# Kernel tuning notes

Measured on AMD Instinct MI355X. Metric: run time of the kernel, lower is better.

The kernel has to match this reference:

```python
import jax, jax.numpy as jnp
import numpy as np

N_NODES = 50000
N_EDGES = 800000
D = 128  # node_feat_size == edge_hidden_size


def setup_inputs() -> dict:
    key = jax.random.key(0)
    ks = jax.random.split(key, 10)
    return {
        "edge_logits": jax.random.normal(ks[0], (N_EDGES, 1), jnp.float32),
        "node_feats": jax.random.normal(ks[1], (N_NODES, D), jnp.float32),
        "src": jax.random.randint(ks[2], (N_EDGES,), 0, N_NODES),
        "dst": jax.random.randint(ks[3], (N_EDGES,), 0, N_NODES),
        "W_proj": jax.random.normal(ks[4], (D, D), jnp.float32) * 0.05,
        "b_proj": jax.random.normal(ks[5], (D,), jnp.float32) * 0.05,
        "W_ih": jax.random.normal(ks[6], (3 * D, D), jnp.float32) * 0.05,
        "b_ih": jax.random.normal(ks[7], (3 * D,), jnp.float32) * 0.05,
        "W_hh": jax.random.normal(ks[8], (3 * D, D), jnp.float32) * 0.05,
        "b_hh": jax.random.normal(ks[9], (3 * D,), jnp.float32) * 0.05,
    }


def reference(edge_logits, node_feats, src, dst, W_proj, b_proj, W_ih, b_ih, W_hh, b_hh):
    N = node_feats.shape[0]
    # --- edge softmax: normalize logits over incoming edges of each dst node ---
    emax = jax.ops.segment_max(edge_logits, dst, num_segments=N)      # [N,1]
    ex = jnp.exp(edge_logits - emax[dst])                             # [E,1]
    esum = jax.ops.segment_sum(ex, dst, num_segments=N)               # [N,1]
    a = ex / esum[dst]                                                # [E,1]
    # --- project nodes (dropout=0 -> identity), gather-multiply-scatter ---
    hv = node_feats @ W_proj.T + b_proj                               # [N,D]
    msg = hv[src] * a                                                 # [E,D]
    c = jax.ops.segment_sum(msg, dst, num_segments=N)                 # [N,D]
    context = jax.nn.elu(c)
    # --- GRUCell(input=context, hidden=node_feats), torch semantics ---
    gi = context @ W_ih.T + b_ih                                      # [N,3D]
    gh = node_feats @ W_hh.T + b_hh                                   # [N,3D]
    i_r, i_z, i_n = jnp.split(gi, 3, axis=-1)
    h_r, h_z, h_n = jnp.split(gh, 3, axis=-1)
    r = jax.nn.sigmoid(i_r + h_r)
    z = jax.nn.sigmoid(i_z + h_z)
    n = jnp.tanh(i_n + r * h_n)
    h_new = (1.0 - z) * n + z * node_feats
    return jax.nn.relu(h_new)
```

## Files before the change

### kernel.cpp

```cpp
#include <hip/hip_runtime.h>
#include <hip/hip_fp16.h>
#include <math.h>

#define NN 50000
#define NE 800000
#define DD 128
#define SLOT 64
#define NXCD 8
#define DRANGE 6250
#define FILLB 1568
#define PROJB 782
#define AGGR_IDX 1563

typedef short bf16x8 __attribute__((ext_vector_type(8)));
typedef float f32x4 __attribute__((ext_vector_type(4)));
typedef unsigned uint4v __attribute__((ext_vector_type(4)));

#define GLOAD_LDS16(gp, lp) \
    __builtin_amdgcn_global_load_lds((const __attribute__((address_space(1))) void*)(gp), \
                                     (__attribute__((address_space(3))) void*)(lp), 16, 0, 0)

__device__ __forceinline__ unsigned short f2bf(float x) {
    unsigned u = __float_as_uint(x);
    unsigned r = (u + 0x7FFFu + ((u >> 16) & 1u)) >> 16;
    return (unsigned short)r;
}
__device__ __forceinline__ float bf2f(unsigned short b) {
    return __uint_as_float(((unsigned)b) << 16);
}
__device__ __forceinline__ unsigned pack2(float x, float y) {
    return (unsigned)f2bf(x) | ((unsigned)f2bf(y) << 16);
}
__device__ __forceinline__ unsigned short f2h(float x) {
    _Float16 h = (_Float16)x;
    return *reinterpret_cast<unsigned short*>(&h);
}
__device__ __forceinline__ float h2f(unsigned short u) {
    _Float16 h = *reinterpret_cast<_Float16*>(&u);
    return (float)h;
}
__device__ __forceinline__ float fsig(float x) { return 1.f / (1.f + __expf(-x)); }
__device__ __forceinline__ float ftanh(float x) { return 1.f - 2.f / (__expf(2.f * x) + 1.f); }

__device__ __forceinline__ float wbig_val(const float* Wih, const float* Whh, int r, int c) {
    if (r < 256)  return (c < 128) ? Wih[r * 128 + c] : Whh[r * 128 + (c - 128)];
    if (r < 384)  return (c < 128) ? Wih[r * 128 + c] : 0.f;
    return (c < 128) ? 0.f : Whh[(r - 128) * 128 + (c - 128)];
}

__global__ __launch_bounds__(256) void k_wprep(const float* __restrict__ Wp,
                                               const float* __restrict__ Wih,
                                               const float* __restrict__ bih,
                                               const float* __restrict__ Whh,
                                               const float* __restrict__ bhh,
                                               int* __restrict__ cnt,
                                               unsigned short* __restrict__ Wfrag,
                                               unsigned short* __restrict__ Wpfrag,
                                               float* __restrict__ bbig) {
    int idx = blockIdx.x * 256 + threadIdx.x;
    if (idx < NN) cnt[idx] = 0;
    if (idx < 512 * 256) {
        int e = idx & 7, lane = (idx >> 3) & 63, ct = (idx >> 9) & 31, ks = idx >> 14;
        int r = ct * 16 + (lane & 15);
        int k = ks * 32 + (lane >> 4) * 8 + e;
        Wfrag[idx] = f2bf(wbig_val(Wih, Whh, r, k));
    } else if (idx < 512 * 256 + 128 * 128) {
        int i = idx - 512 * 256;
        int e = i & 7, lane = (i >> 3) & 63, ct = (i >> 9) & 7, ks = i >> 12;
        int r = ct * 16 + (lane & 15);
        int k = ks * 32 + (lane >> 4) * 8 + e;
        Wpfrag[i] = f2bf(Wp[r * 128 + k]);
    } else if (idx < 512 * 256 + 128 * 128 + 512) {
        int j = idx - (512 * 256 + 128 * 128);
        float v;
        if (j < 256)      v = bih[j] + bhh[j];
        else if (j < 384) v = bih[j];
        else              v = bhh[j - 128];
        bbig[j] = v;
    }
}

__device__ __forceinline__ void fill_one(const float* __restrict__ logits,
                                         const int* __restrict__ src,
                                         int* __restrict__ cnt,
                                         unsigned* __restrict__ csr,
                                         int e, int d) {
    unsigned v = (unsigned)(unsigned short)src[e] |
                 ((unsigned)f2h(__expf(logits[e])) << 16);
    int p = atomicAdd(&cnt[d], 1);
    if (p < SLOT) csr[(size_t)d * SLOT + p] = v;
}

__global__ __launch_bounds__(256, 2) void k_fillproj(const float* __restrict__ logits,
                                                     const int* __restrict__ src,
                                                     const int* __restrict__ dst,
                                                     int* __restrict__ cnt,
                                                     unsigned* __restrict__ csr,
                                                     const float* __restrict__ nf,
                                                     const unsigned short* __restrict__ Wpfrag,
                                                     const float* __restrict__ bp,
                                                     unsigned short* __restrict__ hvb,
                                                     unsigned short* __restrict__ nfb) {
    __shared__ unsigned short Bs[2][8 * 64 * 8];
    if (blockIdx.x < FILLB) {
        const int g = blockIdx.x & 7;
        const int chunk = blockIdx.x >> 3;
        const int dlo = g * DRANGE;
        const int dhi = min(dlo + DRANGE, NN);
#pragma unroll
        for (int i = 0; i < 4; i++) {
            int e4 = chunk * 4096 + i * 1024 + (int)threadIdx.x * 4;
            if (e4 + 3 < NE) {
                int4 d = *(const int4*)(dst + e4);
                if (d.x >= dlo && d.x < dhi) fill_one(logits, src, cnt, csr, e4 + 0, d.x);
                if (d.y >= dlo && d.y < dhi) fill_one(logits, src, cnt, csr, e4 + 1, d.y);
                if (d.z >= dlo && d.z < dhi) fill_one(logits, src, cnt, csr, e4 + 2, d.z);
                if (d.w >= dlo && d.w < dhi) fill_one(logits, src, cnt, csr, e4 + 3, d.w);
            } else {
                for (int k = 0; k < 4; k++) {
                    int e = e4 + k;
                    if (e < NE) {
                        int dd = dst[e];
                        if (dd >= dlo && dd < dhi) fill_one(logits, src, cnt, csr, e, dd);
                    }
                }
            }
        }
        return;
    }
    const int bid = blockIdx.x - FILLB;
    const int t = threadIdx.x;
    const int w = t >> 6;
    const int lane = t & 63;
    const int row0 = bid * 64 + w * 16;
    const int rowA = min(row0 + (lane & 15), NN - 1);
    const int koff = (lane >> 4) * 8;

    bf16x8 a[4];
#pragma unroll
    for (int ks = 0; ks < 4; ks++) {
        const float* p = nf + (size_t)rowA * DD + ks * 32 + koff;
        float4 v0 = *(const float4*)(p);
        float4 v1 = *(const float4*)(p + 4);
        uint4v pk = {pack2(v0.x, v0.y), pack2(v0.z, v0.w),
                     pack2(v1.x, v1.y), pack2(v1.z, v1.w)};
        *reinterpret_cast<uint4v*>(nfb + (size_t)rowA * DD + ks * 32 + koff) = pk;
        a[ks] = *reinterpret_cast<bf16x8*>(&pk);
    }

    f32x4 acc[8];
#pragma unroll
    for (int i = 0; i < 8; i++) acc[i] = (f32x4){0.f, 0.f, 0.f, 0.f};

#pragma unroll
    for (int i = 0; i < 2; i++)
        GLOAD_LDS16(Wpfrag + (size_t)(i * 256 + t) * 8, &Bs[0][(i * 256 + t) * 8]);
    __syncthreads();

#pragma unroll
    for (int ks = 0; ks < 4; ks++) {
        const int cur = ks & 1;
        if (ks < 3) {
#pragma unroll
            for (int i = 0; i < 2; i++)
                GLOAD_LDS16(Wpfrag + (size_t)(ks + 1) * 4096 + (i * 256 + t) * 8,
                            &Bs[cur ^ 1][(i * 256 + t) * 8]);
        }
#pragma unroll
        for (int ct = 0; ct < 8; ct++) {
            bf16x8 b = *reinterpret_cast<const bf16x8*>(&Bs[cur][(ct * 64 + lane) * 8]);
            acc[ct] = __builtin_amdgcn_mfma_f32_16x16x32_bf16(a[ks], b, acc[ct], 0, 0, 0);
        }
        __syncthreads();
    }
#pragma unroll
    for (int ct = 0; ct < 8; ct++) {
        int j = ct * 16 + (lane & 15);
        float bj = bp[j];
#pragma unroll
        for (int reg = 0; reg < 4; reg++) {
            int row = row0 + (lane >> 4) * 4 + reg;
            if (row < NN) hvb[(size_t)row * DD + j] = f2bf(acc[ct][reg] + bj);
        }
    }
}

__global__ __launch_bounds__(256) void k_aggr(const int* __restrict__ cnt,
                                              const unsigned* __restrict__ csr,
                                              const unsigned* __restrict__ hvb,
                                              unsigned* __restrict__ ctx_out) {
    const int g = blockIdx.x & 7;
    const int idx = blockIdx.x >> 3;
    const int n = g * DRANGE + idx * 4 + (threadIdx.x >> 6);
    const int l = threadIdx.x & 63;
    if (n >= (g + 1) * DRANGE || n >= NN) return;
    const int beg = n * SLOT;
    const int deg = min(cnt[n], SLOT);
    const int end = beg + deg;
    float ax = 0.f, ay = 0.f, es = 0.f;
    int e = beg;
    for (; e + 16 <= end; e += 16) {
        unsigned c[16], h[16];
#pragma unroll
        for (int i = 0; i < 16; i++) c[i] = csr[e + i];
#pragma unroll
        for (int i = 0; i < 16; i++) h[i] = hvb[(size_t)(c[i] & 0xFFFF) * 64 + l];
#pragma unroll
        for (int i = 0; i < 16; i++) {
            float a = h2f((unsigned short)(c[i] >> 16));
            es += a;
            ax += a * bf2f((unsigned short)(h[i] & 0xFFFF));
            ay += a * bf2f((unsigned short)(h[i] >> 16));
        }
    }
    for (; e + 4 <= end; e += 4) {
        unsigned c[4], h[4];
#pragma unroll
        for (int i = 0; i < 4; i++) c[i] = csr[e + i];
#pragma unroll
        for (int i = 0; i < 4; i++) h[i] = hvb[(size_t)(c[i] & 0xFFFF) * 64 + l];
#pragma unroll
        for (int i = 0; i < 4; i++) {
            float a = h2f((unsigned short)(c[i] >> 16));
            es += a;
            ax += a * bf2f((unsigned short)(h[i] & 0xFFFF));
            ay += a * bf2f((unsigned short)(h[i] >> 16));
        }
    }
    for (; e < end; e++) {
        unsigned c = csr[e];
        float a = h2f((unsigned short)(c >> 16));
        unsigned hv2 = hvb[(size_t)(c & 0xFFFF) * 64 + l];
        es += a;
        ax += a * bf2f((unsigned short)(hv2 & 0xFFFF));
        ay += a * bf2f((unsigned short)(hv2 >> 16));
    }
    float vx = 0.f, vy = 0.f;
    if (deg > 0) {
        float inv = 1.f / es;
        vx = ax * inv; vy = ay * inv;
        vx = vx > 0.f ? vx : expm1f(vx);
        vy = vy > 0.f ? vy : expm1f(vy);
    }
    ctx_out[(size_t)n * 128 + l] = pack2(vx, vy);
}

__global__ __launch_bounds__(256, 2) void k_gru(const unsigned short* __restrict__ nfb,
                                                const unsigned short* __restrict__ Wfrag,
                                                const float* __restrict__ bbig,
                                                float* __restrict__ out) {
    __shared__ unsigned short Bs[2][4 * 4 * 64 * 8];
    const int t = threadIdx.x;
    const int w = t >> 6;
    const int lane = t & 63;
    const int jblk = blockIdx.x & 1;
    const int row0 = (blockIdx.x >> 1) * 64 + w * 16;
    const int rowA = min(row0 + (lane & 15), NN - 1);
    const int koff = (lane >> 4) * 8;
    const unsigned short* ctxo = (const unsigned short*)out;

    bf16x8 a[8];
#pragma unroll
    for (int ks = 0; ks < 4; ks++)
        a[ks] = *reinterpret_cast<const bf16x8*>(ctxo + (size_t)rowA * 256 + ks * 32 + koff);
#pragma unroll
    for (int ks = 0; ks < 4; ks++)
        a[4 + ks] = *reinterpret_cast<const bf16x8*>(nfb + (size_t)rowA * DD + ks * 32 + koff);

    f32x4 acc[16];
#pragma unroll
    for (int i = 0; i < 16; i++) acc[i] = (f32x4){0.f, 0.f, 0.f, 0.f};

#pragma unroll
    for (int g = 0; g < 4; g++)
        GLOAD_LDS16(Wfrag + (size_t)(g * 8 + jblk * 4) * 512 + t * 8,
                    &Bs[0][g * 2048 + t * 8]);
    __syncthreads();

#pragma unroll
    for (int ks = 0; ks < 8; ks++) {
        const int cur = ks & 1;
        if (ks < 7) {
#pragma unroll
            for (int g = 0; g < 4; g++)
                GLOAD_LDS16(Wfrag + (size_t)(ks + 1) * 16384 +
                                (size_t)(g * 8 + jblk * 4) * 512 + t * 8,
                            &Bs[cur ^ 1][g * 2048 + t * 8]);
        }
#pragma unroll
        for (int q = 0; q < 16; q++) {
            bf16x8 b = *reinterpret_cast<const bf16x8*>(&Bs[cur][q * 512 + lane * 8]);
            acc[q] = __builtin_amdgcn_mfma_f32_16x16x32_bf16(a[ks], b, acc[q], 0, 0, 0);
        }
        __syncthreads();
    }

#pragma unroll
    for (int ctl = 0; ctl < 4; ctl++) {
        int j = jblk * 64 + ctl * 16 + (lane & 15);
        float bR = bbig[j];
        float bZ = bbig[128 + j];
        float bI = bbig[256 + j];
        float bH = bbig[384 + j];
#pragma unroll
        for (int reg = 0; reg < 4; reg++) {
            int row = row0 + (lane >> 4) * 4 + reg;
            if (row < NN) {
                float r = fsig(acc[ctl][reg] + bR);
                float z = fsig(acc[4 + ctl][reg] + bZ);
                float nn = ftanh(acc[8 + ctl][reg] + bI + r * (acc[12 + ctl][reg] + bH));
                float hp = bf2f(nfb[(size_t)row * DD + j]);
                float h = (1.f - z) * nn + z * hp;
                out[(size_t)row * DD + j] = fmaxf(h, 0.f);
            }
        }
    }
}

extern "C" void kernel_launch(void* const* d_in, const int* in_sizes, int n_in,
                              void* d_out, int out_size, void* d_ws, size_t ws_size,
                              hipStream_t stream) {
    const float* edge_logits = (const float*)d_in[0];
    const float* node_feats  = (const float*)d_in[1];
    const int*   src         = (const int*)d_in[2];
    const int*   dst         = (const int*)d_in[3];
    const float* Wp          = (const float*)d_in[4];
    const float* bp          = (const float*)d_in[5];
    const float* Wih         = (const float*)d_in[6];
    const float* bih         = (const float*)d_in[7];
    const float* Whh         = (const float*)d_in[8];
    const float* bhh         = (const float*)d_in[9];
    float* out = (float*)d_out;

    char* ws = (char*)d_ws;
    int*            cnt     = (int*)(ws);
    float*          bbig    = (float*)(ws + 512 * 1024);
    unsigned short* Wpfrag  = (unsigned short*)(ws + 1024 * 1024);
    unsigned short* Wfrag   = (unsigned short*)(ws + 1024 * 1024 + 64 * 1024);
    unsigned*       csr     = (unsigned*)(ws + 2 * 1024 * 1024);
    unsigned short* hvb     = (unsigned short*)(ws + 15 * 1024 * 1024);
    unsigned short* nfb     = (unsigned short*)(ws + 28 * 1024 * 1024);

    k_wprep<<<578, 256, 0, stream>>>(Wp, Wih, bih, Whh, bhh, cnt, Wfrag, Wpfrag, bbig);
    k_fillproj<<<FILLB + PROJB, 256, 0, stream>>>(
        edge_logits, src, dst, cnt, csr, node_feats, Wpfrag, bp, hvb, nfb);
    k_aggr<<<NXCD * AGGR_IDX, 256, 0, stream>>>(cnt, csr, (const unsigned*)hvb, (unsigned*)out);
    k_gru<<<((NN + 63) / 64) * 2, 256, 0, stream>>>((const unsigned short*)nfb, Wfrag, bbig, out);
}
```

Measured before the change: 128.9 us.

## Split node range into halves and software-pipeline fill, aggregate and GRU stages

The graph work is split into two node halves so that each launch overlaps independent stages: fill of the first half runs with the projection, fill of the second half with aggregation of the first, aggregation of the second half with GRU on the early rows, and finally the remaining GRU rows. Each fill pass now rescans the whole dst array while keeping only its own dst range. Loads of dst and node features become nontemporal. The aim is to hide launch gaps and tail imbalance between dependent kernels. The cost is an extra full pass over dst and src/logits, plus an extra launch.

```diff
diff --git a/kernel.cpp b/kernel.cpp
--- a/kernel.cpp
+++ b/kernel.cpp
@@ -7,14 +7,19 @@
 #define DD 128
 #define SLOT 64
 #define NXCD 8
-#define DRANGE 6250
+#define HALF 25000
+#define GR 3125
 #define FILLB 1568
 #define PROJB 782
-#define AGGR_IDX 1563
+#define AGGRB 6256
+#define GRUA 780
+#define GRUB 784
 
 typedef short bf16x8 __attribute__((ext_vector_type(8)));
 typedef float f32x4 __attribute__((ext_vector_type(4)));
 typedef unsigned uint4v __attribute__((ext_vector_type(4)));
+typedef int int4v __attribute__((ext_vector_type(4)));
+typedef float float4v __attribute__((ext_vector_type(4)));
 
 #define GLOAD_LDS16(gp, lp) \
     __builtin_amdgcn_global_load_lds((const __attribute__((address_space(1))) void*)(gp), \
@@ -91,44 +96,44 @@
     if (p < SLOT) csr[(size_t)d * SLOT + p] = v;
 }
 
-__global__ __launch_bounds__(256, 2) void k_fillproj(const float* __restrict__ logits,
-                                                     const int* __restrict__ src,
-                                                     const int* __restrict__ dst,
-                                                     int* __restrict__ cnt,
-                                                     unsigned* __restrict__ csr,
-                                                     const float* __restrict__ nf,
-                                                     const unsigned short* __restrict__ Wpfrag,
-                                                     const float* __restrict__ bp,
-                                                     unsigned short* __restrict__ hvb,
-                                                     unsigned short* __restrict__ nfb) {
-    __shared__ unsigned short Bs[2][8 * 64 * 8];
-    if (blockIdx.x < FILLB) {
-        const int g = blockIdx.x & 7;
-        const int chunk = blockIdx.x >> 3;
-        const int dlo = g * DRANGE;
-        const int dhi = min(dlo + DRANGE, NN);
-#pragma unroll
-        for (int i = 0; i < 4; i++) {
-            int e4 = chunk * 4096 + i * 1024 + (int)threadIdx.x * 4;
-            if (e4 + 3 < NE) {
-                int4 d = *(const int4*)(dst + e4);
-                if (d.x >= dlo && d.x < dhi) fill_one(logits, src, cnt, csr, e4 + 0, d.x);
-                if (d.y >= dlo && d.y < dhi) fill_one(logits, src, cnt, csr, e4 + 1, d.y);
-                if (d.z >= dlo && d.z < dhi) fill_one(logits, src, cnt, csr, e4 + 2, d.z);
-                if (d.w >= dlo && d.w < dhi) fill_one(logits, src, cnt, csr, e4 + 3, d.w);
-            } else {
-                for (int k = 0; k < 4; k++) {
-                    int e = e4 + k;
-                    if (e < NE) {
-                        int dd = dst[e];
-                        if (dd >= dlo && dd < dhi) fill_one(logits, src, cnt, csr, e, dd);
-                    }
+__device__ __forceinline__ void fill_body(int bid, int h,
+                                          const float* __restrict__ logits,
+                                          const int* __restrict__ src,
+                                          const int* __restrict__ dst,
+                                          int* __restrict__ cnt,
+                                          unsigned* __restrict__ csr) {
+    const int g = bid & 7;
+    const int chunk = bid >> 3;
+    const int dlo = h * HALF + g * GR;
+    const int dhi = dlo + GR;
+#pragma unroll
+    for (int i = 0; i < 4; i++) {
+        int e4 = chunk * 4096 + i * 1024 + (int)threadIdx.x * 4;
+        if (e4 + 3 < NE) {
+            int4v d = __builtin_nontemporal_load((const int4v*)(dst + e4));
+            if (d.x >= dlo && d.x < dhi) fill_one(logits, src, cnt, csr, e4 + 0, d.x);
+            if (d.y >= dlo && d.y < dhi) fill_one(logits, src, cnt, csr, e4 + 1, d.y);
+            if (d.z >= dlo && d.z < dhi) fill_one(logits, src, cnt, csr, e4 + 2, d.z);
+            if (d.w >= dlo && d.w < dhi) fill_one(logits, src, cnt, csr, e4 + 3, d.w);
+        } else {
+            for (int k = 0; k < 4; k++) {
+                int e = e4 + k;
+                if (e < NE) {
+                    int dd = dst[e];
+                    if (dd >= dlo && dd < dhi) fill_one(logits, src, cnt, csr, e, dd);
                 }
             }
         }
-        return;
-    }
-    const int bid = blockIdx.x - FILLB;
+    }
+}
+
+__device__ __forceinline__ void proj_body(int bid,
+                                          const float* __restrict__ nf,
+                                          const unsigned short* __restrict__ Wpfrag,
+                                          const float* __restrict__ bp,
+                                          unsigned short* __restrict__ hvb,
+                                          unsigned short* __restrict__ nfb) {
+    __shared__ unsigned short Bs[2][8 * 64 * 8];
     const int t = threadIdx.x;
     const int w = t >> 6;
     const int lane = t & 63;
@@ -140,8 +145,8 @@
 #pragma unroll
     for (int ks = 0; ks < 4; ks++) {
         const float* p = nf + (size_t)rowA * DD + ks * 32 + koff;
-        float4 v0 = *(const float4*)(p);
-        float4 v1 = *(const float4*)(p + 4);
+        float4v v0 = __builtin_nontemporal_load((const float4v*)p);
+        float4v v1 = __builtin_nontemporal_load((const float4v*)(p + 4));
         uint4v pk = {pack2(v0.x, v0.y), pack2(v0.z, v0.w),
                      pack2(v1.x, v1.y), pack2(v1.z, v1.w)};
         *reinterpret_cast<uint4v*>(nfb + (size_t)rowA * DD + ks * 32 + koff) = pk;
@@ -185,46 +190,48 @@
     }
 }
 
-__global__ __launch_bounds__(256) void k_aggr(const int* __restrict__ cnt,
-                                              const unsigned* __restrict__ csr,
-                                              const unsigned* __restrict__ hvb,
-                                              unsigned* __restrict__ ctx_out) {
-    const int g = blockIdx.x & 7;
-    const int idx = blockIdx.x >> 3;
-    const int n = g * DRANGE + idx * 4 + (threadIdx.x >> 6);
+__device__ __forceinline__ void aggr_body(int bid, int h,
+                                          const int* __restrict__ cnt,
+                                          const unsigned* __restrict__ csr,
+                                          const unsigned* __restrict__ hvb,
+                                          unsigned* __restrict__ ctx_out) {
+    const int g = bid & 7;
+    const int idx = bid >> 3;
+    const int local = idx * 4 + ((int)threadIdx.x >> 6);
     const int l = threadIdx.x & 63;
-    if (n >= (g + 1) * DRANGE || n >= NN) return;
+    if (local >= GR) return;
+    const int n = h * HALF + g * GR + local;
     const int beg = n * SLOT;
     const int deg = min(cnt[n], SLOT);
     const int end = beg + deg;
     float ax = 0.f, ay = 0.f, es = 0.f;
     int e = beg;
     for (; e + 16 <= end; e += 16) {
-        unsigned c[16], h[16];
+        unsigned c[16], hh[16];
 #pragma unroll
         for (int i = 0; i < 16; i++) c[i] = csr[e + i];
 #pragma unroll
-        for (int i = 0; i < 16; i++) h[i] = hvb[(size_t)(c[i] & 0xFFFF) * 64 + l];
+        for (int i = 0; i < 16; i++) hh[i] = hvb[(size_t)(c[i] & 0xFFFF) * 64 + l];
 #pragma unroll
         for (int i = 0; i < 16; i++) {
             float a = h2f((unsigned short)(c[i] >> 16));
             es += a;
-            ax += a * bf2f((unsigned short)(h[i] & 0xFFFF));
-            ay += a * bf2f((unsigned short)(h[i] >> 16));
+            ax += a * bf2f((unsigned short)(hh[i] & 0xFFFF));
+            ay += a * bf2f((unsigned short)(hh[i] >> 16));
         }
     }
     for (; e + 4 <= end; e += 4) {
-        unsigned c[4], h[4];
+        unsigned c[4], hh[4];
 #pragma unroll
         for (int i = 0; i < 4; i++) c[i] = csr[e + i];
 #pragma unroll
-        for (int i = 0; i < 4; i++) h[i] = hvb[(size_t)(c[i] & 0xFFFF) * 64 + l];
+        for (int i = 0; i < 4; i++) hh[i] = hvb[(size_t)(c[i] & 0xFFFF) * 64 + l];
 #pragma unroll
         for (int i = 0; i < 4; i++) {
             float a = h2f((unsigned short)(c[i] >> 16));
             es += a;
-            ax += a * bf2f((unsigned short)(h[i] & 0xFFFF));
-            ay += a * bf2f((unsigned short)(h[i] >> 16));
+            ax += a * bf2f((unsigned short)(hh[i] & 0xFFFF));
+            ay += a * bf2f((unsigned short)(hh[i] >> 16));
         }
     }
     for (; e < end; e++) {
@@ -245,16 +252,17 @@
     ctx_out[(size_t)n * 128 + l] = pack2(vx, vy);
 }
 
-__global__ __launch_bounds__(256, 2) void k_gru(const unsigned short* __restrict__ nfb,
-                                                const unsigned short* __restrict__ Wfrag,
-                                                const float* __restrict__ bbig,
-                                                float* __restrict__ out) {
+__device__ __forceinline__ void gru_body(int gbid,
+                                         const unsigned short* __restrict__ nfb,
+                                         const unsigned short* __restrict__ Wfrag,
+                                         const float* __restrict__ bbig,
+                                         float* __restrict__ out) {
     __shared__ unsigned short Bs[2][4 * 4 * 64 * 8];
     const int t = threadIdx.x;
     const int w = t >> 6;
     const int lane = t & 63;
-    const int jblk = blockIdx.x & 1;
-    const int row0 = (blockIdx.x >> 1) * 64 + w * 16;
+    const int jblk = gbid & 1;
+    const int row0 = (gbid >> 1) * 64 + w * 16;
     const int rowA = min(row0 + (lane & 15), NN - 1);
     const int koff = (lane >> 4) * 8;
     const unsigned short* ctxo = (const unsigned short*)out;
@@ -315,6 +323,51 @@
             }
         }
     }
+}
+
+
+__global__ __launch_bounds__(256, 2) void k_s2(const float* __restrict__ logits,
+                                               const int* __restrict__ src,
+                                               const int* __restrict__ dst,
+                                               int* __restrict__ cnt,
+                                               unsigned* __restrict__ csr,
+                                               const float* __restrict__ nf,
+                                               const unsigned short* __restrict__ Wpfrag,
+                                               const float* __restrict__ bp,
+                                               unsigned short* __restrict__ hvb,
+                                               unsigned short* __restrict__ nfb) {
+    if (blockIdx.x < FILLB) fill_body(blockIdx.x, 0, logits, src, dst, cnt, csr);
+    else proj_body(blockIdx.x - FILLB, nf, Wpfrag, bp, hvb, nfb);
+}
+
+__global__ __launch_bounds__(256) void k_s3(const float* __restrict__ logits,
+                                            const int* __restrict__ src,
+                                            const int* __restrict__ dst,
+                                            int* __restrict__ cnt,
+                                            unsigned* __restrict__ csr,
+                                            const unsigned* __restrict__ hvb,
+                                            unsigned* __restrict__ ctx_out) {
+    if (blockIdx.x < FILLB) fill_body(blockIdx.x, 1, logits, src, dst, cnt, csr);
+    else aggr_body(blockIdx.x - FILLB, 0, cnt, (const unsigned*)csr, hvb, ctx_out);
+}
+
+__global__ __launch_bounds__(256, 2) void k_s4(const int* __restrict__ cnt,
+                                               const unsigned* __restrict__ csr,
+                                               const unsigned* __restrict__ hvb,
+                                               unsigned* __restrict__ ctx_out,
+                                               const unsigned short* __restrict__ nfb,
+                                               const unsigned short* __restrict__ Wfrag,
+                                               const float* __restrict__ bbig,
+                                               float* __restrict__ out) {
+    if (blockIdx.x < AGGRB) aggr_body(blockIdx.x, 1, cnt, csr, hvb, ctx_out);
+    else gru_body(blockIdx.x - AGGRB, nfb, Wfrag, bbig, out);
+}
+
+__global__ __launch_bounds__(256, 2) void k_s5(const unsigned short* __restrict__ nfb,
+                                               const unsigned short* __restrict__ Wfrag,
+                                               const float* __restrict__ bbig,
+                                               float* __restrict__ out) {
+    gru_body(GRUA + (int)blockIdx.x, nfb, Wfrag, bbig, out);
 }
 
 extern "C" void kernel_launch(void* const* d_in, const int* in_sizes, int n_in,
@@ -342,8 +395,11 @@
     unsigned short* nfb     = (unsigned short*)(ws + 28 * 1024 * 1024);
 
     k_wprep<<<578, 256, 0, stream>>>(Wp, Wih, bih, Whh, bhh, cnt, Wfrag, Wpfrag, bbig);
-    k_fillproj<<<FILLB + PROJB, 256, 0, stream>>>(
-        edge_logits, src, dst, cnt, csr, node_feats, Wpfrag, bp, hvb, nfb);
-    k_aggr<<<NXCD * AGGR_IDX, 256, 0, stream>>>(cnt, csr, (const unsigned*)hvb, (unsigned*)out);
-    k_gru<<<((NN + 63) / 64) * 2, 256, 0, stream>>>((const unsigned short*)nfb, Wfrag, bbig, out);
-}
+    k_s2<<<FILLB + PROJB, 256, 0, stream>>>(edge_logits, src, dst, cnt, csr,
+                                            node_feats, Wpfrag, bp, hvb, nfb);
+    k_s3<<<FILLB + AGGRB, 256, 0, stream>>>(edge_logits, src, dst, cnt, csr,
+                                            (const unsigned*)hvb, (unsigned*)out);
+    k_s4<<<AGGRB + GRUA, 256, 0, stream>>>(cnt, csr, (const unsigned*)hvb, (unsigned*)out,
+                                           (const unsigned short*)nfb, Wfrag, bbig, out);
+    k_s5<<<GRUB, 256, 0, stream>>>((const unsigned short*)nfb, Wfrag, bbig, out);
+}
```

Result: slower. 163.2 us (+26.6%).
